# Kernel optimization log

Hardware: AMD Instinct MI355X
Metric: run time of the kernel (lower is better)

Reference implementation:

```python
import jax, jax.numpy as jnp
import numpy as np

N = 20000      # nodes
E = 320000     # directed edges (before self loops)
IN_DIM = 384
D = 256        # hidden_dim
H = 4          # heads
C = D // H     # per-head channels = 64
L = 3          # layers
NEG_SLOPE = 0.2
LN_EPS = 1e-5


def setup_inputs() -> dict:
    key = jax.random.key(0)
    ks = jax.random.split(key, 8)
    return {
        "x": jax.random.normal(ks[0], (N, IN_DIM), jnp.float32),
        "edge_index": jax.random.randint(ks[1], (2, E), 0, N),
        "w_in": jax.random.normal(ks[2], (IN_DIM, D), jnp.float32) * 0.05,
        "b_in": jnp.zeros((D,), jnp.float32),
        "wl": jax.random.normal(ks[3], (L, D, D), jnp.float32) * 0.05,
        "wr": jax.random.normal(ks[4], (L, D, D), jnp.float32) * 0.05,
        "att": jax.random.normal(ks[5], (L, H, C), jnp.float32) * 0.05,
        "bias": jnp.zeros((L, D), jnp.float32),
        "ln_g": jnp.ones((L, D), jnp.float32),
        "ln_b": jnp.zeros((L, D), jnp.float32),
    }


def _layernorm(h, g, b):
    mu = jnp.mean(h, axis=-1, keepdims=True)
    var = jnp.mean(jnp.square(h - mu), axis=-1, keepdims=True)
    return (h - mu) * jax.lax.rsqrt(var + LN_EPS) * g + b


def _gatv2(h, src, dst, Wl, Wr, a, b):
    # PyG GATv2Conv, concat=True, eval mode (no dropout), self-loops already in src/dst.
    xl = (h @ Wl).reshape(N, H, C)   # source transform (lin_l)
    xr = (h @ Wr).reshape(N, H, C)   # target transform (lin_r)
    x_j = xl[src]                    # [E', H, C] gathered source messages
    e = jnp.einsum('ehc,hc->eh', jax.nn.leaky_relu(x_j + xr[dst], NEG_SLOPE), a)
    # segment softmax over edges grouped by destination node
    m = jax.ops.segment_max(e, dst, num_segments=N)
    e = jnp.exp(e - m[dst])
    s = jax.ops.segment_sum(e, dst, num_segments=N)
    alpha = e / (s[dst] + 1e-16)     # [E', H]
    out = jax.ops.segment_sum(x_j * alpha[:, :, None], dst, num_segments=N)
    return out.reshape(N, D) + b


def reference(x, edge_index, w_in, b_in, wl, wr, att, bias, ln_g, ln_b):
    loops = jnp.arange(N, dtype=edge_index.dtype)
    src = jnp.concatenate([edge_index[0], loops])
    dst = jnp.concatenate([edge_index[1], loops])
    h = x @ w_in + b_in
    for l in range(L):
        h_new = _layernorm(_gatv2(h, src, dst, wl[l], wr[l], att[l], bias[l]),
                           ln_g[l], ln_b[l])
        h = h + h_new  # shapes always match since concat output == hidden_dim
    norm = jnp.linalg.norm(h, axis=-1, keepdims=True)
    return h / jnp.maximum(norm, 1e-12)
```

## Files before the change

### kernel.cpp

```cpp
#include <hip/hip_runtime.h>
#include <math.h>

#define N_NODES 20000
#define E_EDGES 320000
#define E_TOT   (E_EDGES + N_NODES)
#define IN_DIM  384
#define DIM     256
#define LAYERS  3
#define NEG_SLOPE 0.2f
#define LN_EPS 1e-5f

typedef unsigned short u16;
typedef unsigned int u32;
typedef __attribute__((ext_vector_type(8))) short short8;
typedef __attribute__((ext_vector_type(8))) __bf16 bf16x8;
typedef __attribute__((ext_vector_type(4))) float f32x4;

__device__ inline u16 f2bf(float f) {
    u32 u = __builtin_bit_cast(u32, f);
    return (u16)((u + 0x7fffu + ((u >> 16) & 1u)) >> 16);
}
__device__ inline float bf2f(u16 s) {
    u32 u = (u32)s << 16;
    return __builtin_bit_cast(float, u);
}
__device__ inline float4 cvt4(ushort4 u) {
    return make_float4(bf2f(u.x), bf2f(u.y), bf2f(u.z), bf2f(u.w));
}

__device__ inline f32x4 mfma_bf16(short8 a, short8 b, f32x4 c) {
    return __builtin_amdgcn_mfma_f32_16x16x32_bf16(
        __builtin_bit_cast(bf16x8, a), __builtin_bit_cast(bf16x8, b), c, 0, 0, 0);
}

__device__ inline void gl_lds16(const u16* g, u16* l) {
    __builtin_amdgcn_global_load_lds(
        (const __attribute__((address_space(1))) u32*)g,
        (__attribute__((address_space(3))) u32*)l, 16, 0, 0);
}

__global__ void count_kernel(const int* __restrict__ ei, int* __restrict__ counts) {
    int e = blockIdx.x * 256 + threadIdx.x;
    if (e >= E_TOT) return;
    int d = (e < E_EDGES) ? ei[E_EDGES + e] : (e - E_EDGES);
    atomicAdd(&counts[d], 1);
}

__global__ __launch_bounds__(1024) void scan_kernel(const int* __restrict__ counts,
                                                    int* __restrict__ row_ptr) {
    __shared__ int sums[1024];
    const int t = threadIdx.x;
    const int CH = (N_NODES + 1023) / 1024;
    int base = t * CH;
    int local = 0;
    for (int i = 0; i < CH; ++i) {
        int idx = base + i;
        if (idx < N_NODES) local += counts[idx];
    }
    sums[t] = local;
    __syncthreads();
    for (int off = 1; off < 1024; off <<= 1) {
        int v = (t >= off) ? sums[t - off] : 0;
        __syncthreads();
        sums[t] += v;
        __syncthreads();
    }
    int run = (t == 0) ? 0 : sums[t - 1];
    for (int i = 0; i < CH; ++i) {
        int idx = base + i;
        if (idx < N_NODES) { row_ptr[idx] = run; run += counts[idx]; }
    }
    if (t == 1023) row_ptr[N_NODES] = sums[1023];
}

__global__ void scatter_kernel(const int* __restrict__ ei, const int* __restrict__ row_ptr,
                               int* __restrict__ cursor, int* __restrict__ csr_src) {
    int e = blockIdx.x * 256 + threadIdx.x;
    if (e >= E_TOT) return;
    int s, d;
    if (e < E_EDGES) { s = ei[e]; d = ei[E_EDGES + e]; }
    else { s = e - E_EDGES; d = s; }
    int pos = row_ptr[d] + atomicAdd(&cursor[d], 1);
    csr_src[pos] = s;
}

__global__ void convert_bf16(const float* __restrict__ in, u16* __restrict__ out, int n4) {
    int i = blockIdx.x * 256 + threadIdx.x;
    if (i >= n4) return;
    float4 v = reinterpret_cast<const float4*>(in)[i];
    reinterpret_cast<ushort4*>(out)[i] =
        make_ushort4(f2bf(v.x), f2bf(v.y), f2bf(v.z), f2bf(v.w));
}

#define W_IN_ELEMS (IN_DIM * DIM)
#define W_LR_ELEMS (2 * DIM * DIM)
#define W_TOT (W_IN_ELEMS + LAYERS * W_LR_ELEMS)
__global__ void convert_weights(const float* __restrict__ w_in, const float* __restrict__ wl,
                                const float* __restrict__ wr, u16* __restrict__ out) {
    int idx = blockIdx.x * 256 + threadIdx.x;
    if (idx >= W_TOT) return;
    float v;
    if (idx < W_IN_ELEMS) {
        int n = idx / IN_DIM, k = idx % IN_DIM;
        v = w_in[k * DIM + n];
    } else {
        int j = idx - W_IN_ELEMS;
        int l = j / W_LR_ELEMS;
        int r = j % W_LR_ELEMS;
        int n = r >> 8, k = r & 255;
        const float* W = (n < DIM) ? wl : wr;
        v = W[l * DIM * DIM + k * DIM + (n & 255)];
    }
    out[idx] = f2bf(v);
}

#define BM 128
#define BN 128
#define BK 64
template <int K, int MODE>
__global__ __launch_bounds__(256) void gemm_mfma(
    const u16* __restrict__ A, const u16* __restrict__ B,
    const float* __restrict__ bias,
    float* __restrict__ C, u16* __restrict__ Cbf,
    int M, int ldc) {
    __shared__ u16 lds[2][2][BM * BK];
    const int tid = threadIdx.x;
    const int w = tid >> 6, lane = tid & 63;
    const int wm = w >> 1, wn = w & 1;
    const int bm = blockIdx.y * BM, bn = blockIdx.x * BN;
    const int fr = lane & 15, q = lane >> 4;

    f32x4 acc[4][4] = {};

    const int s_row = tid >> 3, s_blk = tid & 7;
    constexpr int NT = K / BK;

#pragma unroll
    for (int i = 0; i < 4; ++i) {
        int row = i * 32 + s_row;
        int gcol = ((s_blk ^ (row & 7)) << 3);
        int base = (i * 256 + (tid & ~63)) << 3;
        int ra = min(bm + row, M - 1);
        gl_lds16(A + (size_t)ra * K + gcol, &lds[0][0][base]);
        gl_lds16(B + (size_t)(bn + row) * K + gcol, &lds[0][1][base]);
    }
    __syncthreads();

    for (int t = 0; t < NT; ++t) {
        const int p = t & 1;
        if (t + 1 < NT) {
            const int k0 = (t + 1) * BK;
#pragma unroll
            for (int i = 0; i < 4; ++i) {
                int row = i * 32 + s_row;
                int gcol = ((s_blk ^ (row & 7)) << 3);
                int base = (i * 256 + (tid & ~63)) << 3;
                int ra = min(bm + row, M - 1);
                gl_lds16(A + (size_t)ra * K + k0 + gcol, &lds[p ^ 1][0][base]);
                gl_lds16(B + (size_t)(bn + row) * K + k0 + gcol, &lds[p ^ 1][1][base]);
            }
        }
        short8 a_f[2][4], b_f[2][4];
#pragma unroll
        for (int kk = 0; kk < 2; ++kk) {
#pragma unroll
            for (int mi = 0; mi < 4; ++mi) {
                int row = wm * 64 + mi * 16 + fr;
                a_f[kk][mi] = *reinterpret_cast<const short8*>(
                    &lds[p][0][row * BK + ((((kk << 2) + q) ^ (row & 7)) << 3)]);
            }
#pragma unroll
            for (int ni = 0; ni < 4; ++ni) {
                int row = wn * 64 + ni * 16 + fr;
                b_f[kk][ni] = *reinterpret_cast<const short8*>(
                    &lds[p][1][row * BK + ((((kk << 2) + q) ^ (row & 7)) << 3)]);
            }
        }
#pragma unroll
        for (int kk = 0; kk < 2; ++kk)
#pragma unroll
            for (int mi = 0; mi < 4; ++mi)
#pragma unroll
                for (int ni = 0; ni < 4; ++ni)
                    acc[mi][ni] = mfma_bf16(a_f[kk][mi], b_f[kk][ni], acc[mi][ni]);
        __syncthreads();
    }

#pragma unroll
    for (int mi = 0; mi < 4; ++mi) {
#pragma unroll
        for (int r = 0; r < 4; ++r) {
            int row = bm + wm * 64 + mi * 16 + q * 4 + r;
            if (row >= M) continue;
#pragma unroll
            for (int ni = 0; ni < 4; ++ni) {
                int col = bn + wn * 64 + ni * 16 + fr;
                float v = acc[mi][ni][r];
                if (MODE == 0) {
                    v += bias[col];
                    C[(size_t)row * ldc + col] = v;
                }
                Cbf[(size_t)row * ldc + col] = f2bf(v);
            }
        }
    }
}

template <bool LAST>
__global__ __launch_bounds__(256) void gat_edge(const u16* __restrict__ xlr_bf,
                                                const int* __restrict__ row_ptr,
                                                const int* __restrict__ csr_src,
                                                const float* __restrict__ att,
                                                const float* __restrict__ bias,
                                                const float* __restrict__ ln_g,
                                                const float* __restrict__ ln_b,
                                                float* __restrict__ h,
                                                u16* __restrict__ h_bf,
                                                float* __restrict__ out) {
    const int wave = threadIdx.x >> 6;
    const int lane = threadIdx.x & 63;
    const int node = blockIdx.x * 4 + wave;
    if (node >= N_NODES) return;
    const int c4 = lane << 2;

    const float4 a4  = *reinterpret_cast<const float4*>(att + c4);
    const float4 xr4 = cvt4(*reinterpret_cast<const ushort4*>(
        xlr_bf + (size_t)node * 512 + 256 + c4));

    float sA = 0.f, sB = 0.f;
    float4 accA = make_float4(0.f, 0.f, 0.f, 0.f);
    float4 accB = make_float4(0.f, 0.f, 0.f, 0.f);

    const int e0 = row_ptr[node], e1 = row_ptr[node + 1];
    int e = e0;
    for (; e + 1 < e1; e += 2) {
        int srcA = csr_src[e], srcB = csr_src[e + 1];
        float4 xa = cvt4(*reinterpret_cast<const ushort4*>(xlr_bf + (size_t)srcA * 512 + c4));
        float4 xb = cvt4(*reinterpret_cast<const ushort4*>(xlr_bf + (size_t)srcB * 512 + c4));

        float vax = xa.x + xr4.x; vax = fmaxf(vax, NEG_SLOPE * vax);
        float vay = xa.y + xr4.y; vay = fmaxf(vay, NEG_SLOPE * vay);
        float vaz = xa.z + xr4.z; vaz = fmaxf(vaz, NEG_SLOPE * vaz);
        float vaw = xa.w + xr4.w; vaw = fmaxf(vaw, NEG_SLOPE * vaw);
        float pA = vax * a4.x + vay * a4.y + vaz * a4.z + vaw * a4.w;

        float vbx = xb.x + xr4.x; vbx = fmaxf(vbx, NEG_SLOPE * vbx);
        float vby = xb.y + xr4.y; vby = fmaxf(vby, NEG_SLOPE * vby);
        float vbz = xb.z + xr4.z; vbz = fmaxf(vbz, NEG_SLOPE * vbz);
        float vbw = xb.w + xr4.w; vbw = fmaxf(vbw, NEG_SLOPE * vbw);
        float pB = vbx * a4.x + vby * a4.y + vbz * a4.z + vbw * a4.w;

        pA += __shfl_xor(pA, 1); pB += __shfl_xor(pB, 1);
        pA += __shfl_xor(pA, 2); pB += __shfl_xor(pB, 2);
        pA += __shfl_xor(pA, 4); pB += __shfl_xor(pB, 4);
        pA += __shfl_xor(pA, 8); pB += __shfl_xor(pB, 8);

        float peA = __expf(pA);
        float peB = __expf(pB);
        sA += peA; sB += peB;
        accA.x = fmaf(peA, xa.x, accA.x);
        accA.y = fmaf(peA, xa.y, accA.y);
        accA.z = fmaf(peA, xa.z, accA.z);
        accA.w = fmaf(peA, xa.w, accA.w);
        accB.x = fmaf(peB, xb.x, accB.x);
        accB.y = fmaf(peB, xb.y, accB.y);
        accB.z = fmaf(peB, xb.z, accB.z);
        accB.w = fmaf(peB, xb.w, accB.w);
    }
    if (e < e1) {
        int src = csr_src[e];
        float4 xa = cvt4(*reinterpret_cast<const ushort4*>(xlr_bf + (size_t)src * 512 + c4));
        float vax = xa.x + xr4.x; vax = fmaxf(vax, NEG_SLOPE * vax);
        float vay = xa.y + xr4.y; vay = fmaxf(vay, NEG_SLOPE * vay);
        float vaz = xa.z + xr4.z; vaz = fmaxf(vaz, NEG_SLOPE * vaz);
        float vaw = xa.w + xr4.w; vaw = fmaxf(vaw, NEG_SLOPE * vaw);
        float pA = vax * a4.x + vay * a4.y + vaz * a4.z + vaw * a4.w;
        pA += __shfl_xor(pA, 1);
        pA += __shfl_xor(pA, 2);
        pA += __shfl_xor(pA, 4);
        pA += __shfl_xor(pA, 8);
        float peA = __expf(pA);
        sA += peA;
        accA.x = fmaf(peA, xa.x, accA.x);
        accA.y = fmaf(peA, xa.y, accA.y);
        accA.z = fmaf(peA, xa.z, accA.z);
        accA.w = fmaf(peA, xa.w, accA.w);
    }
    float s = sA + sB;
    float inv = 1.f / (s + 1e-16f);
    const float4 b4 = *reinterpret_cast<const float4*>(bias + c4);
    float ox = (accA.x + accB.x) * inv + b4.x;
    float oy = (accA.y + accB.y) * inv + b4.y;
    float oz = (accA.z + accB.z) * inv + b4.z;
    float ow = (accA.w + accB.w) * inv + b4.w;

    float lsum = ox + oy + oz + ow;
    float lsq  = ox * ox + oy * oy + oz * oz + ow * ow;
#pragma unroll
    for (int off = 1; off < 64; off <<= 1) {
        lsum += __shfl_xor(lsum, off);
        lsq  += __shfl_xor(lsq, off);
    }
    float mu = lsum * (1.f / 256.f);
    float var = lsq * (1.f / 256.f) - mu * mu;
    float rstd = rsqrtf(var + LN_EPS);
    const float4 g4  = *reinterpret_cast<const float4*>(ln_g + c4);
    const float4 lb4 = *reinterpret_cast<const float4*>(ln_b + c4);
    float4 hv = *reinterpret_cast<const float4*>(h + (size_t)node * DIM + c4);
    hv.x += (ox - mu) * rstd * g4.x + lb4.x;
    hv.y += (oy - mu) * rstd * g4.y + lb4.y;
    hv.z += (oz - mu) * rstd * g4.z + lb4.z;
    hv.w += (ow - mu) * rstd * g4.w + lb4.w;

    if (LAST) {
        float nsq = hv.x * hv.x + hv.y * hv.y + hv.z * hv.z + hv.w * hv.w;
#pragma unroll
        for (int off = 1; off < 64; off <<= 1) nsq += __shfl_xor(nsq, off);
        float ninv = 1.f / fmaxf(sqrtf(nsq), 1e-12f);
        float4 o = make_float4(hv.x * ninv, hv.y * ninv, hv.z * ninv, hv.w * ninv);
        *reinterpret_cast<float4*>(out + (size_t)node * DIM + c4) = o;
    } else {
        *reinterpret_cast<float4*>(h + (size_t)node * DIM + c4) = hv;
        *reinterpret_cast<ushort4*>(h_bf + (size_t)node * DIM + c4) =
            make_ushort4(f2bf(hv.x), f2bf(hv.y), f2bf(hv.z), f2bf(hv.w));
    }
}

extern "C" void kernel_launch(void* const* d_in, const int* in_sizes, int n_in,
                              void* d_out, int out_size, void* d_ws, size_t ws_size,
                              hipStream_t stream) {
    const float* x    = (const float*)d_in[0];
    const int*   ei   = (const int*)d_in[1];
    const float* w_in = (const float*)d_in[2];
    const float* b_in = (const float*)d_in[3];
    const float* wl   = (const float*)d_in[4];
    const float* wr   = (const float*)d_in[5];
    const float* att  = (const float*)d_in[6];
    const float* bias = (const float*)d_in[7];
    const float* ln_g = (const float*)d_in[8];
    const float* ln_b = (const float*)d_in[9];

    char* p = (char*)d_ws;
    float* h      = (float*)p;            p += (size_t)N_NODES * DIM * 4;
    u16*   h_bf   = (u16*)p;              p += (size_t)N_NODES * DIM * 2;
    u16*   xlr_bf = (u16*)p;              p += (size_t)N_NODES * 512 * 2;
    u16*   w_bf   = (u16*)p;              p += (size_t)W_TOT * 2;
    int* row_ptr  = (int*)p;              p += (N_NODES + 1) * 4;
    int* counts   = (int*)p;              p += N_NODES * 4;
    int* cursor   = (int*)p;              p += N_NODES * 4;
    int* csr_src  = (int*)p;

    u16* x_bf = xlr_bf;

    hipMemsetAsync(counts, 0, sizeof(int) * 2 * N_NODES, stream);
    count_kernel<<<(E_TOT + 255) / 256, 256, 0, stream>>>(ei, counts);
    scan_kernel<<<1, 1024, 0, stream>>>(counts, row_ptr);
    scatter_kernel<<<(E_TOT + 255) / 256, 256, 0, stream>>>(ei, row_ptr, cursor, csr_src);

    {
        int n4 = N_NODES * IN_DIM / 4;
        convert_bf16<<<(n4 + 255) / 256, 256, 0, stream>>>(x, x_bf, n4);
        convert_weights<<<(W_TOT + 255) / 256, 256, 0, stream>>>(w_in, wl, wr, w_bf);
    }

    gemm_mfma<IN_DIM, 0><<<dim3(DIM / BN, (N_NODES + BM - 1) / BM), 256, 0, stream>>>(
        x_bf, w_bf, b_in, h, h_bf, N_NODES, DIM);

    for (int l = 0; l < LAYERS; ++l) {
        const u16* wlr = w_bf + W_IN_ELEMS + (size_t)l * W_LR_ELEMS;
        gemm_mfma<DIM, 1><<<dim3(512 / BN, (N_NODES + BM - 1) / BM), 256, 0, stream>>>(
            h_bf, wlr, nullptr, nullptr, xlr_bf, N_NODES, 512);
        if (l < LAYERS - 1) {
            gat_edge<false><<<(N_NODES + 3) / 4, 256, 0, stream>>>(
                xlr_bf, row_ptr, csr_src,
                att + (size_t)l * DIM, bias + (size_t)l * DIM,
                ln_g + (size_t)l * DIM, ln_b + (size_t)l * DIM,
                h, h_bf, nullptr);
        } else {
            gat_edge<true><<<(N_NODES + 3) / 4, 256, 0, stream>>>(
                xlr_bf, row_ptr, csr_src,
                att + (size_t)l * DIM, bias + (size_t)l * DIM,
                ln_g + (size_t)l * DIM, ln_b + (size_t)l * DIM,
                h, h_bf, (float*)d_out);
        }
    }
}
```

Baseline: 257.5 us.

## Fuse prep kernels, drop fp32 residual, batch edge index loads, remap GEMM tiles

Merges count, x conversion and weight conversion into one prep kernel. Removes the fp32 residual buffer h, so the residual is kept only in bf16, which cuts memory traffic but loses precision across layers. The edge loop now loads 64 source indices per wave at once, shares them with shuffles, and issues 4 gathers in flight using packed float2 math. GEMM blocks are remapped in an XCD-aware round-robin order to improve L2 locality.

```diff
diff --git a/kernel.cpp b/kernel.cpp
--- a/kernel.cpp
+++ b/kernel.cpp
@@ -24,8 +24,14 @@
     u32 u = (u32)s << 16;
     return __builtin_bit_cast(float, u);
 }
-__device__ inline float4 cvt4(ushort4 u) {
-    return make_float4(bf2f(u.x), bf2f(u.y), bf2f(u.z), bf2f(u.w));
+
+__device__ inline float2 f2add(float2 a, float2 b) { return make_float2(a.x + b.x, a.y + b.y); }
+__device__ inline float2 f2mul(float2 a, float2 b) { return make_float2(a.x * b.x, a.y * b.y); }
+__device__ inline float2 f2fma(float2 a, float2 b, float2 c) {
+    return make_float2(fmaf(a.x, b.x, c.x), fmaf(a.y, b.y, c.y));
+}
+__device__ inline float2 f2max(float2 a, float2 b) {
+    return make_float2(fmaxf(a.x, b.x), fmaxf(a.y, b.y));
 }
 
 __device__ inline f32x4 mfma_bf16(short8 a, short8 b, f32x4 c) {
@@ -39,11 +45,44 @@
         (__attribute__((address_space(3))) u32*)l, 16, 0, 0);
 }
 
-__global__ void count_kernel(const int* __restrict__ ei, int* __restrict__ counts) {
-    int e = blockIdx.x * 256 + threadIdx.x;
-    if (e >= E_TOT) return;
-    int d = (e < E_EDGES) ? ei[E_EDGES + e] : (e - E_EDGES);
-    atomicAdd(&counts[d], 1);
+#define W_IN_ELEMS (IN_DIM * DIM)
+#define W_LR_ELEMS (2 * DIM * DIM)
+#define W_TOT (W_IN_ELEMS + LAYERS * W_LR_ELEMS)
+
+#define N4X (N_NODES * IN_DIM / 4)
+__global__ void prep_kernel(const int* __restrict__ ei, int* __restrict__ counts,
+                            const float* __restrict__ x, u16* __restrict__ x_bf,
+                            const float* __restrict__ w_in, const float* __restrict__ wl,
+                            const float* __restrict__ wr, u16* __restrict__ w_out) {
+    int tid = blockIdx.x * 256 + threadIdx.x;
+    if (tid < E_TOT) {
+        int d = (tid < E_EDGES) ? ei[E_EDGES + tid] : (tid - E_EDGES);
+        atomicAdd(&counts[d], 1);
+        return;
+    }
+    tid -= E_TOT;
+    if (tid < N4X) {
+        float4 v = reinterpret_cast<const float4*>(x)[tid];
+        reinterpret_cast<ushort4*>(x_bf)[tid] =
+            make_ushort4(f2bf(v.x), f2bf(v.y), f2bf(v.z), f2bf(v.w));
+        return;
+    }
+    tid -= N4X;
+    if (tid < W_TOT) {
+        float v;
+        if (tid < W_IN_ELEMS) {
+            int n = tid / IN_DIM, k = tid % IN_DIM;
+            v = w_in[k * DIM + n];
+        } else {
+            int j = tid - W_IN_ELEMS;
+            int l = j / W_LR_ELEMS;
+            int r = j % W_LR_ELEMS;
+            int n = r >> 8, k = r & 255;
+            const float* W = (n < DIM) ? wl : wr;
+            v = W[l * DIM * DIM + k * DIM + (n & 255)];
+        }
+        w_out[tid] = f2bf(v);
+    }
 }
 
 __global__ __launch_bounds__(1024) void scan_kernel(const int* __restrict__ counts,
@@ -84,50 +123,25 @@
     csr_src[pos] = s;
 }
 
-__global__ void convert_bf16(const float* __restrict__ in, u16* __restrict__ out, int n4) {
-    int i = blockIdx.x * 256 + threadIdx.x;
-    if (i >= n4) return;
-    float4 v = reinterpret_cast<const float4*>(in)[i];
-    reinterpret_cast<ushort4*>(out)[i] =
-        make_ushort4(f2bf(v.x), f2bf(v.y), f2bf(v.z), f2bf(v.w));
-}
-
-#define W_IN_ELEMS (IN_DIM * DIM)
-#define W_LR_ELEMS (2 * DIM * DIM)
-#define W_TOT (W_IN_ELEMS + LAYERS * W_LR_ELEMS)
-__global__ void convert_weights(const float* __restrict__ w_in, const float* __restrict__ wl,
-                                const float* __restrict__ wr, u16* __restrict__ out) {
-    int idx = blockIdx.x * 256 + threadIdx.x;
-    if (idx >= W_TOT) return;
-    float v;
-    if (idx < W_IN_ELEMS) {
-        int n = idx / IN_DIM, k = idx % IN_DIM;
-        v = w_in[k * DIM + n];
-    } else {
-        int j = idx - W_IN_ELEMS;
-        int l = j / W_LR_ELEMS;
-        int r = j % W_LR_ELEMS;
-        int n = r >> 8, k = r & 255;
-        const float* W = (n < DIM) ? wl : wr;
-        v = W[l * DIM * DIM + k * DIM + (n & 255)];
-    }
-    out[idx] = f2bf(v);
-}
-
 #define BM 128
 #define BN 128
 #define BK 64
-template <int K, int MODE>
+template <int K, bool BIAS, int NX, int NTOT>
 __global__ __launch_bounds__(256) void gemm_mfma(
     const u16* __restrict__ A, const u16* __restrict__ B,
-    const float* __restrict__ bias,
-    float* __restrict__ C, u16* __restrict__ Cbf,
+    const float* __restrict__ bias, u16* __restrict__ Cbf,
     int M, int ldc) {
     __shared__ u16 lds[2][2][BM * BK];
     const int tid = threadIdx.x;
     const int w = tid >> 6, lane = tid & 63;
     const int wm = w >> 1, wn = w & 1;
-    const int bm = blockIdx.y * BM, bn = blockIdx.x * BN;
+
+    int lin = blockIdx.y * NX + blockIdx.x;
+    constexpr int q8 = NTOT >> 3, r8 = NTOT & 7;
+    int k8 = lin & 7, j8 = lin >> 3;
+    int bid2 = k8 * q8 + min(k8, r8) + j8;
+    const int bm = (bid2 / NX) * BM, bn = (bid2 % NX) * BN;
+
     const int fr = lane & 15, q = lane >> 4;
 
     f32x4 acc[4][4] = {};
@@ -196,10 +210,7 @@
             for (int ni = 0; ni < 4; ++ni) {
                 int col = bn + wn * 64 + ni * 16 + fr;
                 float v = acc[mi][ni][r];
-                if (MODE == 0) {
-                    v += bias[col];
-                    C[(size_t)row * ldc + col] = v;
-                }
+                if (BIAS) v += bias[col];
                 Cbf[(size_t)row * ldc + col] = f2bf(v);
             }
         }
@@ -214,7 +225,6 @@
                                                 const float* __restrict__ bias,
                                                 const float* __restrict__ ln_g,
                                                 const float* __restrict__ ln_b,
-                                                float* __restrict__ h,
                                                 u16* __restrict__ h_bf,
                                                 float* __restrict__ out) {
     const int wave = threadIdx.x >> 6;
@@ -223,79 +233,68 @@
     if (node >= N_NODES) return;
     const int c4 = lane << 2;
 
-    const float4 a4  = *reinterpret_cast<const float4*>(att + c4);
-    const float4 xr4 = cvt4(*reinterpret_cast<const ushort4*>(
-        xlr_bf + (size_t)node * 512 + 256 + c4));
+    const float4 a4 = *reinterpret_cast<const float4*>(att + c4);
+    const float2 a01 = make_float2(a4.x, a4.y), a23 = make_float2(a4.z, a4.w);
+    const ushort4 uxr = *reinterpret_cast<const ushort4*>(xlr_bf + (size_t)node * 512 + 256 + c4);
+    const float2 xr01 = make_float2(bf2f(uxr.x), bf2f(uxr.y));
+    const float2 xr23 = make_float2(bf2f(uxr.z), bf2f(uxr.w));
+    const float2 k02 = make_float2(NEG_SLOPE, NEG_SLOPE);
 
     float sA = 0.f, sB = 0.f;
-    float4 accA = make_float4(0.f, 0.f, 0.f, 0.f);
-    float4 accB = make_float4(0.f, 0.f, 0.f, 0.f);
-
-    const int e0 = row_ptr[node], e1 = row_ptr[node + 1];
-    int e = e0;
-    for (; e + 1 < e1; e += 2) {
-        int srcA = csr_src[e], srcB = csr_src[e + 1];
-        float4 xa = cvt4(*reinterpret_cast<const ushort4*>(xlr_bf + (size_t)srcA * 512 + c4));
-        float4 xb = cvt4(*reinterpret_cast<const ushort4*>(xlr_bf + (size_t)srcB * 512 + c4));
-
-        float vax = xa.x + xr4.x; vax = fmaxf(vax, NEG_SLOPE * vax);
-        float vay = xa.y + xr4.y; vay = fmaxf(vay, NEG_SLOPE * vay);
-        float vaz = xa.z + xr4.z; vaz = fmaxf(vaz, NEG_SLOPE * vaz);
-        float vaw = xa.w + xr4.w; vaw = fmaxf(vaw, NEG_SLOPE * vaw);
-        float pA = vax * a4.x + vay * a4.y + vaz * a4.z + vaw * a4.w;
-
-        float vbx = xb.x + xr4.x; vbx = fmaxf(vbx, NEG_SLOPE * vbx);
-        float vby = xb.y + xr4.y; vby = fmaxf(vby, NEG_SLOPE * vby);
-        float vbz = xb.z + xr4.z; vbz = fmaxf(vbz, NEG_SLOPE * vbz);
-        float vbw = xb.w + xr4.w; vbw = fmaxf(vbw, NEG_SLOPE * vbw);
-        float pB = vbx * a4.x + vby * a4.y + vbz * a4.z + vbw * a4.w;
-
-        pA += __shfl_xor(pA, 1); pB += __shfl_xor(pB, 1);
-        pA += __shfl_xor(pA, 2); pB += __shfl_xor(pB, 2);
-        pA += __shfl_xor(pA, 4); pB += __shfl_xor(pB, 4);
-        pA += __shfl_xor(pA, 8); pB += __shfl_xor(pB, 8);
-
-        float peA = __expf(pA);
-        float peB = __expf(pB);
-        sA += peA; sB += peB;
-        accA.x = fmaf(peA, xa.x, accA.x);
-        accA.y = fmaf(peA, xa.y, accA.y);
-        accA.z = fmaf(peA, xa.z, accA.z);
-        accA.w = fmaf(peA, xa.w, accA.w);
-        accB.x = fmaf(peB, xb.x, accB.x);
-        accB.y = fmaf(peB, xb.y, accB.y);
-        accB.z = fmaf(peB, xb.z, accB.z);
-        accB.w = fmaf(peB, xb.w, accB.w);
-    }
-    if (e < e1) {
-        int src = csr_src[e];
-        float4 xa = cvt4(*reinterpret_cast<const ushort4*>(xlr_bf + (size_t)src * 512 + c4));
-        float vax = xa.x + xr4.x; vax = fmaxf(vax, NEG_SLOPE * vax);
-        float vay = xa.y + xr4.y; vay = fmaxf(vay, NEG_SLOPE * vay);
-        float vaz = xa.z + xr4.z; vaz = fmaxf(vaz, NEG_SLOPE * vaz);
-        float vaw = xa.w + xr4.w; vaw = fmaxf(vaw, NEG_SLOPE * vaw);
-        float pA = vax * a4.x + vay * a4.y + vaz * a4.z + vaw * a4.w;
-        pA += __shfl_xor(pA, 1);
-        pA += __shfl_xor(pA, 2);
-        pA += __shfl_xor(pA, 4);
-        pA += __shfl_xor(pA, 8);
-        float peA = __expf(pA);
-        sA += peA;
-        accA.x = fmaf(peA, xa.x, accA.x);
-        accA.y = fmaf(peA, xa.y, accA.y);
-        accA.z = fmaf(peA, xa.z, accA.z);
-        accA.w = fmaf(peA, xa.w, accA.w);
-    }
+    float2 aA01 = make_float2(0.f, 0.f), aA23 = aA01, aB01 = aA01, aB23 = aA01;
+
+    const int e0 = row_ptr[node];
+    const int d = row_ptr[node + 1] - e0;
+
+    for (int base = 0; base < d; base += 64) {
+        const int rem = min(d - base, 64);
+        const int idx = base + lane;
+        const int my_src = (idx < d) ? csr_src[e0 + idx] : node;
+        for (int k = 0; k < rem; k += 4) {
+            ushort4 uu[4];
+#pragma unroll
+            for (int j = 0; j < 4; ++j) {
+                int s = __shfl(my_src, k + j);
+                uu[j] = *reinterpret_cast<const ushort4*>(xlr_bf + (size_t)s * 512 + c4);
+            }
+#pragma unroll
+            for (int j = 0; j < 4; ++j) {
+                float2 v01 = make_float2(bf2f(uu[j].x), bf2f(uu[j].y));
+                float2 v23 = make_float2(bf2f(uu[j].z), bf2f(uu[j].w));
+                float2 t01 = f2add(v01, xr01), t23 = f2add(v23, xr23);
+                float2 l01 = f2max(t01, f2mul(t01, k02));
+                float2 l23 = f2max(t23, f2mul(t23, k02));
+                float2 dd = f2fma(l01, a01, f2mul(l23, a23));
+                float p = dd.x + dd.y;
+                p += __shfl_xor(p, 1);
+                p += __shfl_xor(p, 2);
+                p += __shfl_xor(p, 4);
+                p += __shfl_xor(p, 8);
+                float pe = (k + j < rem) ? __expf(p) : 0.f;
+                float2 pe2 = make_float2(pe, pe);
+                if (j & 1) {
+                    sB += pe;
+                    aB01 = f2fma(pe2, v01, aB01);
+                    aB23 = f2fma(pe2, v23, aB23);
+                } else {
+                    sA += pe;
+                    aA01 = f2fma(pe2, v01, aA01);
+                    aA23 = f2fma(pe2, v23, aA23);
+                }
+            }
+        }
+    }
+
     float s = sA + sB;
     float inv = 1.f / (s + 1e-16f);
+    float2 inv2 = make_float2(inv, inv);
+    float2 acc01 = f2add(aA01, aB01), acc23 = f2add(aA23, aB23);
     const float4 b4 = *reinterpret_cast<const float4*>(bias + c4);
-    float ox = (accA.x + accB.x) * inv + b4.x;
-    float oy = (accA.y + accB.y) * inv + b4.y;
-    float oz = (accA.z + accB.z) * inv + b4.z;
-    float ow = (accA.w + accB.w) * inv + b4.w;
-
-    float lsum = ox + oy + oz + ow;
-    float lsq  = ox * ox + oy * oy + oz * oz + ow * ow;
+    float2 o01 = f2fma(acc01, inv2, make_float2(b4.x, b4.y));
+    float2 o23 = f2fma(acc23, inv2, make_float2(b4.z, b4.w));
+
+    float lsum = o01.x + o01.y + o23.x + o23.y;
+    float lsq = o01.x * o01.x + o01.y * o01.y + o23.x * o23.x + o23.y * o23.y;
 #pragma unroll
     for (int off = 1; off < 64; off <<= 1) {
         lsum += __shfl_xor(lsum, off);
@@ -306,23 +305,28 @@
     float rstd = rsqrtf(var + LN_EPS);
     const float4 g4  = *reinterpret_cast<const float4*>(ln_g + c4);
     const float4 lb4 = *reinterpret_cast<const float4*>(ln_b + c4);
-    float4 hv = *reinterpret_cast<const float4*>(h + (size_t)node * DIM + c4);
-    hv.x += (ox - mu) * rstd * g4.x + lb4.x;
-    hv.y += (oy - mu) * rstd * g4.y + lb4.y;
-    hv.z += (oz - mu) * rstd * g4.z + lb4.z;
-    hv.w += (ow - mu) * rstd * g4.w + lb4.w;
+    float2 mu2 = make_float2(-mu, -mu), rstd2 = make_float2(rstd, rstd);
+
+    const ushort4 uh = *reinterpret_cast<const ushort4*>(h_bf + (size_t)node * DIM + c4);
+    float2 h01 = make_float2(bf2f(uh.x), bf2f(uh.y));
+    float2 h23 = make_float2(bf2f(uh.z), bf2f(uh.w));
+    float2 n01 = f2fma(f2mul(f2add(o01, mu2), rstd2), make_float2(g4.x, g4.y),
+                       make_float2(lb4.x, lb4.y));
+    float2 n23 = f2fma(f2mul(f2add(o23, mu2), rstd2), make_float2(g4.z, g4.w),
+                       make_float2(lb4.z, lb4.w));
+    h01 = f2add(h01, n01);
+    h23 = f2add(h23, n23);
 
     if (LAST) {
-        float nsq = hv.x * hv.x + hv.y * hv.y + hv.z * hv.z + hv.w * hv.w;
+        float nsq = h01.x * h01.x + h01.y * h01.y + h23.x * h23.x + h23.y * h23.y;
 #pragma unroll
         for (int off = 1; off < 64; off <<= 1) nsq += __shfl_xor(nsq, off);
         float ninv = 1.f / fmaxf(sqrtf(nsq), 1e-12f);
-        float4 o = make_float4(hv.x * ninv, hv.y * ninv, hv.z * ninv, hv.w * ninv);
+        float4 o = make_float4(h01.x * ninv, h01.y * ninv, h23.x * ninv, h23.y * ninv);
         *reinterpret_cast<float4*>(out + (size_t)node * DIM + c4) = o;
     } else {
-        *reinterpret_cast<float4*>(h + (size_t)node * DIM + c4) = hv;
         *reinterpret_cast<ushort4*>(h_bf + (size_t)node * DIM + c4) =
-            make_ushort4(f2bf(hv.x), f2bf(hv.y), f2bf(hv.z), f2bf(hv.w));
+            make_ushort4(f2bf(h01.x), f2bf(h01.y), f2bf(h23.x), f2bf(h23.y));
     }
 }
 
@@ -341,7 +345,6 @@
     const float* ln_b = (const float*)d_in[9];
 
     char* p = (char*)d_ws;
-    float* h      = (float*)p;            p += (size_t)N_NODES * DIM * 4;
     u16*   h_bf   = (u16*)p;              p += (size_t)N_NODES * DIM * 2;
     u16*   xlr_bf = (u16*)p;              p += (size_t)N_NODES * 512 * 2;
     u16*   w_bf   = (u16*)p;              p += (size_t)W_TOT * 2;
@@ -353,35 +356,34 @@
     u16* x_bf = xlr_bf;
 
     hipMemsetAsync(counts, 0, sizeof(int) * 2 * N_NODES, stream);
-    count_kernel<<<(E_TOT + 255) / 256, 256, 0, stream>>>(ei, counts);
+    {
+        int total = E_TOT + N4X + W_TOT;
+        prep_kernel<<<(total + 255) / 256, 256, 0, stream>>>(
+            ei, counts, x, x_bf, w_in, wl, wr, w_bf);
+    }
     scan_kernel<<<1, 1024, 0, stream>>>(counts, row_ptr);
     scatter_kernel<<<(E_TOT + 255) / 256, 256, 0, stream>>>(ei, row_ptr, cursor, csr_src);
 
-    {
-        int n4 = N_NODES * IN_DIM / 4;
-        convert_bf16<<<(n4 + 255) / 256, 256, 0, stream>>>(x, x_bf, n4);
-        convert_weights<<<(W_TOT + 255) / 256, 256, 0, stream>>>(w_in, wl, wr, w_bf);
-    }
-
-    gemm_mfma<IN_DIM, 0><<<dim3(DIM / BN, (N_NODES + BM - 1) / BM), 256, 0, stream>>>(
-        x_bf, w_bf, b_in, h, h_bf, N_NODES, DIM);
+    constexpr int NYT = (N_NODES + BM - 1) / BM;
+    gemm_mfma<IN_DIM, true, 2, 2 * NYT><<<dim3(2, NYT), 256, 0, stream>>>(
+        x_bf, w_bf, b_in, h_bf, N_NODES, DIM);
 
     for (int l = 0; l < LAYERS; ++l) {
         const u16* wlr = w_bf + W_IN_ELEMS + (size_t)l * W_LR_ELEMS;
-        gemm_mfma<DIM, 1><<<dim3(512 / BN, (N_NODES + BM - 1) / BM), 256, 0, stream>>>(
-            h_bf, wlr, nullptr, nullptr, xlr_bf, N_NODES, 512);
+        gemm_mfma<DIM, false, 4, 4 * NYT><<<dim3(4, NYT), 256, 0, stream>>>(
+            h_bf, wlr, nullptr, xlr_bf, N_NODES, 512);
         if (l < LAYERS - 1) {
             gat_edge<false><<<(N_NODES + 3) / 4, 256, 0, stream>>>(
                 xlr_bf, row_ptr, csr_src,
                 att + (size_t)l * DIM, bias + (size_t)l * DIM,
                 ln_g + (size_t)l * DIM, ln_b + (size_t)l * DIM,
-                h, h_bf, nullptr);
+                h_bf, nullptr);
         } else {
             gat_edge<true><<<(N_NODES + 3) / 4, 256, 0, stream>>>(
                 xlr_bf, row_ptr, csr_src,
                 att + (size_t)l * DIM, bias + (size_t)l * DIM,
                 ln_g + (size_t)l * DIM, ln_b + (size_t)l * DIM,
-                h, h_bf, (float*)d_out);
-        }
-    }
-}
+                h_bf, (float*)d_out);
+        }
+    }
+}
```

Result: no change. 260.1 us (+1.0%).
